# Optimization experiments

Measured on AMD Instinct MI355X. Metric: run time of the kernel, lower is better.

## Reference

```python
import math
import jax, jax.numpy as jnp
import numpy as np


def _expmap0(u):
    # geoopt Lorentz (k=1) expmap0 followed by projection back onto the hyperboloid.
    # Minkowski norm of the tangent input (geoopt clamps at 1e-8 before sqrt).
    u0 = u[..., :1]
    us = u[..., 1:]
    mink = -u0 * u0 + jnp.sum(us * us, axis=-1, keepdims=True)
    nomin = jnp.sqrt(jnp.maximum(mink, 1e-8))
    r = jnp.sinh(nomin) * u / nomin
    space = r[..., 1:]
    time = jnp.sqrt(1.0 + jnp.sum(space * space, axis=-1, keepdims=True))  # project()
    return jnp.concatenate([time, space], axis=-1)


def setup_inputs() -> dict:
    key = jax.random.key(0)
    B, T, E, H = 2, 1024, 1024, 16
    ks = jax.random.split(key, 8)
    s = 0.02
    return {
        "x": jax.random.normal(ks[0], (B, T, E), jnp.float32),
        "Wqkv": jax.random.normal(ks[1], (3 * E, E), jnp.float32) * s,
        "bqkv": jnp.zeros((3 * E,), jnp.float32),
        "Wout": jax.random.normal(ks[2], (E, E), jnp.float32) * s,
        "bout": jnp.zeros((E,), jnp.float32),
        "Wimp": jax.random.normal(ks[3], (1, E), jnp.float32) * s,
        "bimp": jnp.zeros((1,), jnp.float32),
        "Walpha": jax.random.normal(ks[4], (H, E), jnp.float32) * s,
        "balpha": jnp.zeros((H,), jnp.float32),
        "spike_threshold": jnp.asarray(0.5, jnp.float32),
        "log_k": jnp.full((H,), 0.54, jnp.float32),
        "qk_scale": jnp.asarray(0.1, jnp.float32),
    }


def reference(x, Wqkv, bqkv, Wout, bout, Wimp, bimp, Walpha, balpha,
              spike_threshold, log_k, qk_scale):
    B, T, C = x.shape
    H = log_k.shape[0]
    D = C // H

    importance = jax.nn.sigmoid(x @ Wimp.T + bimp)          # (B,T,1)
    # torch.tril on the (T,1) trailing dims keeps every element -> no-op mask.
    spikes = (importance > spike_threshold).astype(x.dtype)
    spike_mask = spikes.reshape(B, 1, T, 1)

    alpha = jax.nn.sigmoid(x @ Walpha.T + balpha)           # (B,T,H)
    alpha = jnp.transpose(alpha, (0, 2, 1))[..., None]      # (B,H,T,1)

    qkv = (x @ Wqkv.T + bqkv).reshape(B, T, 3, H, D)
    q = jnp.transpose(qkv[:, :, 0], (0, 2, 1, 3))           # (B,H,T,D)
    k = jnp.transpose(qkv[:, :, 1], (0, 2, 1, 3))
    v = jnp.transpose(qkv[:, :, 2], (0, 2, 1, 3))

    scores_euclid = jnp.einsum('bhtd,bhsd->bhts', q, k) / math.sqrt(D)

    safe_scale = jax.nn.sigmoid(qk_scale) * 1.5
    qn = q / jnp.maximum(jnp.linalg.norm(q, axis=-1, keepdims=True), 1e-12) * safe_scale
    kn = k / jnp.maximum(jnp.linalg.norm(k, axis=-1, keepdims=True), 1e-12) * safe_scale
    q_hyp = _expmap0(qn)
    k_hyp = _expmap0(kn)

    inner = (-jnp.einsum('bhti,bhsi->bhts', q_hyp[..., :1], k_hyp[..., :1])
             + jnp.einsum('bhtd,bhsd->bhts', q_hyp[..., 1:], k_hyp[..., 1:]))
    curv_k = (jax.nn.softplus(log_k) + 1e-6).reshape(1, H, 1, 1)
    mdot = jnp.maximum(-inner, 1.0 + 1e-6)
    dist = jnp.arccosh(mdot)
    scores_hyper = -(dist * dist) / curv_k

    scores = (1.0 - alpha) * scores_euclid + alpha * scores_hyper
    causal = jnp.tril(jnp.ones((T, T), bool))
    scores = jnp.where(causal[None, None], scores, -jnp.inf)

    attn = jax.nn.softmax(scores, axis=-1) * spike_mask     # dropout disabled (eval)
    y = jnp.einsum('bhts,bhsd->bhtd', attn, v)
    y = jnp.transpose(y, (0, 2, 1, 3)).reshape(B, T, C)
    return y @ Wout.T + bout
```

## Files before the change

### kernel.cpp

```cpp
#include <hip/hip_runtime.h>
#include <math.h>

#define B_ 2
#define T_ 1024
#define E_ 1024
#define H_ 16
#define D_ 64
#define M_ (B_*T_)

typedef __bf16 bf16x8 __attribute__((ext_vector_type(8)));
typedef __bf16 bf16x4 __attribute__((ext_vector_type(4)));
typedef float f32x4 __attribute__((ext_vector_type(4)));

__device__ __forceinline__ void* ldsp(__bf16* base, int row, int byte) {
  return (char*)base + row * 128 + (byte ^ ((row & 7) << 4));
}

__device__ __forceinline__ void gload_lds16(const void* g, void* l) {
  __builtin_amdgcn_global_load_lds((const __attribute__((address_space(1))) void*)g,
                                   (__attribute__((address_space(3))) void*)l, 16, 0, 0);
}

#define XV4 524288
#define WQV4 786432
#define WOV4 262144
#define TOTV4 (XV4 + WQV4 + WOV4)
__global__ __launch_bounds__(256) void conv_kernel(
    const float* __restrict__ x, const float* __restrict__ Wqkv,
    const float* __restrict__ Wout,
    __bf16* __restrict__ xb, __bf16* __restrict__ Wqkvb, __bf16* __restrict__ Woutb) {
  for (size_t i = (size_t)blockIdx.x * blockDim.x + threadIdx.x; i < TOTV4;
       i += (size_t)gridDim.x * blockDim.x) {
    const float4* src; __bf16* dst; size_t off;
    if (i < XV4)            { src = (const float4*)x;    dst = xb;    off = i; }
    else if (i < XV4+WQV4)  { src = (const float4*)Wqkv; dst = Wqkvb; off = i - XV4; }
    else                    { src = (const float4*)Wout; dst = Woutb; off = i - XV4 - WQV4; }
    float4 val = src[off];
    bf16x4 o = {(__bf16)val.x, (__bf16)val.y, (__bf16)val.z, (__bf16)val.w};
    *(bf16x4*)(dst + off * 4) = o;
  }
}

__global__ __launch_bounds__(256) void imp_alpha_kernel(
    const float* __restrict__ x,
    const float* __restrict__ Wimp, const float* __restrict__ bimp,
    const float* __restrict__ Walpha, const float* __restrict__ balpha,
    const float* __restrict__ thr_p,
    float* __restrict__ spike, float* __restrict__ alpha) {
  int m = blockIdx.x;
  int tid = threadIdx.x;
  const float* xr = x + (size_t)m * E_;
  float part[17];
#pragma unroll
  for (int i = 0; i < 17; ++i) part[i] = 0.f;
  for (int e = tid; e < E_; e += 256) {
    float xv = xr[e];
    part[16] += xv * Wimp[e];
#pragma unroll
    for (int h = 0; h < 16; ++h) part[h] += xv * Walpha[h * E_ + e];
  }
  __shared__ float red[17][4];
  int lane = tid & 63, wv = tid >> 6;
#pragma unroll
  for (int i = 0; i < 17; ++i) {
    float v = part[i];
    for (int off = 32; off > 0; off >>= 1) v += __shfl_down(v, off, 64);
    if (lane == 0) red[i][wv] = v;
  }
  __syncthreads();
  if (tid < 17) {
    float v = red[tid][0] + red[tid][1] + red[tid][2] + red[tid][3];
    if (tid == 16) {
      float z = v + bimp[0];
      float sig = 1.f / (1.f + expf(-z));
      spike[m] = (sig > thr_p[0]) ? 1.f : 0.f;
    } else {
      float z = v + balpha[tid];
      float a = 1.f / (1.f + expf(-z));
      int b = m >> 10, t = m & (T_ - 1);
      alpha[((size_t)(b * H_ + tid)) * T_ + t] = a;
    }
  }
}

__global__ __launch_bounds__(256) void qkv_gemm_kernel(
    const __bf16* __restrict__ A, const __bf16* __restrict__ Bm,
    const float* __restrict__ bias,
    __bf16* __restrict__ q, __bf16* __restrict__ k, __bf16* __restrict__ v) {
  __shared__ __bf16 As[128 * 32];
  __shared__ __bf16 Bs[128 * 32];
  const int K = E_;
  int tid = threadIdx.x;
  int w = tid >> 6, lane = tid & 63, lr = lane & 15, g = lane >> 4;
  int m0 = blockIdx.y * 128, n0 = blockIdx.x * 128;
  int wr = (w >> 1) * 64, wc = (w & 1) * 64;

  int task0 = tid, task1 = tid + 256;
  int r0s = task0 >> 2, c0s = task0 & 3;
  int r1s = task1 >> 2, c1s = task1 & 3;
  const __bf16* gA0 = A + (size_t)(m0 + r0s) * K + c0s * 8;
  const __bf16* gA1 = A + (size_t)(m0 + r1s) * K + c1s * 8;
  const __bf16* gB0 = Bm + (size_t)(n0 + r0s) * K + c0s * 8;
  const __bf16* gB1 = Bm + (size_t)(n0 + r1s) * K + c1s * 8;
  __bf16* lA0 = As + task0 * 8;
  __bf16* lA1 = As + task1 * 8;
  __bf16* lB0 = Bs + task0 * 8;
  __bf16* lB1 = Bs + task1 * 8;

  f32x4 acc[4][4];
#pragma unroll
  for (int i = 0; i < 4; ++i)
#pragma unroll
    for (int j = 0; j < 4; ++j) acc[i][j] = (f32x4){0.f, 0.f, 0.f, 0.f};

  for (int k0 = 0; k0 < K; k0 += 32) {
    gload_lds16(gA0, lA0); gload_lds16(gA1, lA1);
    gload_lds16(gB0, lB0); gload_lds16(gB1, lB1);
    gA0 += 32; gA1 += 32; gB0 += 32; gB1 += 32;
    __syncthreads();
    bf16x8 af[4], bf[4];
#pragma unroll
    for (int i = 0; i < 4; ++i) af[i] = *(bf16x8*)&As[(wr + i * 16 + lr) * 32 + g * 8];
#pragma unroll
    for (int j = 0; j < 4; ++j) bf[j] = *(bf16x8*)&Bs[(wc + j * 16 + lr) * 32 + g * 8];
#pragma unroll
    for (int i = 0; i < 4; ++i)
#pragma unroll
      for (int j = 0; j < 4; ++j)
        acc[i][j] = __builtin_amdgcn_mfma_f32_16x16x32_bf16(af[i], bf[j], acc[i][j], 0, 0, 0);
    __syncthreads();
  }

#pragma unroll
  for (int i = 0; i < 4; ++i) {
#pragma unroll
    for (int r = 0; r < 4; ++r) {
      int m = m0 + wr + i * 16 + g * 4 + r;
      int b = m >> 10, t = m & (T_ - 1);
#pragma unroll
      for (int j = 0; j < 4; ++j) {
        int n = n0 + wc + j * 16 + lr;
        float val = acc[i][j][r] + bias[n];
        int comp = n >> 10, h = (n >> 6) & 15, d = n & 63;
        __bf16* dst = (comp == 0) ? q : ((comp == 1) ? k : v);
        dst[(((size_t)(b * H_ + h)) * T_ + t) * 64 + d] = (__bf16)val;
      }
    }
  }
}

__global__ __launch_bounds__(256) void hyp_kernel(
    const __bf16* __restrict__ q, const __bf16* __restrict__ k,
    const float* __restrict__ qk_scale_p,
    __bf16* __restrict__ qh, __bf16* __restrict__ khn) {
  int wid = blockIdx.x * 4 + (threadIdx.x >> 6);
  int lane = threadIdx.x & 63;
  int is_k = wid >> 15;
  int row = wid & 32767;
  const __bf16* src = (is_k ? k : q) + (size_t)row * 64;
  float u = (float)src[lane];
  float nsq = u * u;
#pragma unroll
  for (int off = 32; off > 0; off >>= 1) nsq += __shfl_xor(nsq, off, 64);
  float norm = fmaxf(sqrtf(nsq), 1e-12f);
  float ss = 1.5f / (1.f + expf(-qk_scale_p[0]));
  float un = u / norm * ss;
  float s2 = un * un;
  float tot = s2;
#pragma unroll
  for (int off = 32; off > 0; off >>= 1) tot += __shfl_xor(tot, off, 64);
  float un0 = __shfl(un, 0, 64);
  float mink = tot - 2.f * un0 * un0;
  float nomin = sqrtf(fmaxf(mink, 1e-8f));
  float sc = sinhf(nomin) / nomin;
  float r = sc * un;
  float sp2 = (lane == 0) ? 0.f : r * r;
  float sps = sp2;
#pragma unroll
  for (int off = 32; off > 0; off >>= 1) sps += __shfl_xor(sps, off, 64);
  float tm = sqrtf(1.f + sps);
  float outv = (lane == 0) ? tm : r;
  if (is_k && lane != 0) outv = -outv;
  (is_k ? khn : qh)[(size_t)row * 64 + lane] = (__bf16)outv;
}

__global__ __launch_bounds__(256) void attn_kernel(
    const __bf16* __restrict__ q, const __bf16* __restrict__ k, const __bf16* __restrict__ v,
    const __bf16* __restrict__ qh, const __bf16* __restrict__ khn,
    const float* __restrict__ alpha, const float* __restrict__ log_k,
    __bf16* __restrict__ pacc, float* __restrict__ pml) {
  __shared__ __bf16 k_s[64 * 64];
  __shared__ __bf16 kh_s[64 * 64];
  __shared__ __bf16 vt_s[64 * 64];
  __shared__ __bf16 p_s[64 * 64];

  int bid = blockIdx.x;
  int bh = ((bid & 7) << 2) | ((bid >> 3) & 3);
  int rest = bid >> 5;
  int qt = rest & 15;
  int half = rest >> 4;
  int h = bh & 15;
  int t0 = qt * 64;
  int n_st = qt + 1;
  int nh = (n_st + 1) >> 1;
  int s_beg = half ? nh : 0;
  int s_end = half ? n_st : nh;

  int tid = threadIdx.x;
  int w = tid >> 6, lane = tid & 63;
  int lr = lane & 15, g = lane >> 4;
  int trow = w * 16;
  const size_t base = (size_t)bh * T_ * 64;

  const __bf16* qrow = q + base + (size_t)(t0 + trow + lr) * 64;
  const __bf16* qhrow = qh + base + (size_t)(t0 + trow + lr) * 64;
  bf16x8 aq0 = *(const bf16x8*)(qrow + g * 8);
  bf16x8 aq1 = *(const bf16x8*)(qrow + 32 + g * 8);
  bf16x8 ah0 = *(const bf16x8*)(qhrow + g * 8);
  bf16x8 ah1 = *(const bf16x8*)(qhrow + 32 + g * 8);

  float curv = log1pf(expf(log_k[h])) + 1e-6f;
  float hc = 0.69314718056f / curv;
  const float ec = 0.18033688f;
  int tg[4]; float al[4];
#pragma unroll
  for (int r = 0; r < 4; ++r) {
    tg[r] = t0 + trow + g * 4 + r;
    al[r] = alpha[(size_t)bh * T_ + tg[r]];
  }

  float m_r[4] = {-1e30f, -1e30f, -1e30f, -1e30f};
  float l_r[4] = {0.f, 0.f, 0.f, 0.f};
  f32x4 acc[4];
#pragma unroll
  for (int n = 0; n < 4; ++n) acc[n] = (f32x4){0.f, 0.f, 0.f, 0.f};

  for (int st = s_beg; st < s_end; ++st) {
    int s0 = st * 64;
    bool diag = (st == n_st - 1);
    __syncthreads();
#pragma unroll
    for (int it = 0; it < 2; ++it) {
      int task = tid + it * 256;
      int row = task >> 3, cj = task & 7;
      bf16x8 a = *(const bf16x8*)(k + base + (size_t)(s0 + row) * 64 + cj * 8);
      bf16x8 c = *(const bf16x8*)(khn + base + (size_t)(s0 + row) * 64 + cj * 8);
      *(bf16x8*)ldsp(k_s, row, cj * 16) = a;
      *(bf16x8*)ldsp(kh_s, row, cj * 16) = c;
    }
#pragma unroll
    for (int it = 0; it < 2; ++it) {
      int task = tid + it * 256;
      int srow = task & 63, dc = task >> 6;
      bf16x8 a = *(const bf16x8*)(v + base + (size_t)(s0 + srow) * 64 + dc * 8);
#pragma unroll
      for (int i = 0; i < 8; ++i)
        *(__bf16*)ldsp(vt_s, dc * 8 + i, srow * 2) = a[i];
    }
    __syncthreads();

    float pv[4][4];
    float pmax[4] = {-1e30f, -1e30f, -1e30f, -1e30f};
#pragma unroll
    for (int j = 0; j < 4; ++j) {
      if (diag && (s0 + j * 16 > t0 + trow + 15)) {
#pragma unroll
        for (int r = 0; r < 4; ++r) pv[j][r] = -1e30f;
        continue;
      }
      bf16x8 bk0 = *(bf16x8*)ldsp(k_s, j * 16 + lr, g * 16);
      bf16x8 bk1 = *(bf16x8*)ldsp(k_s, j * 16 + lr, 64 + g * 16);
      f32x4 z = {0.f, 0.f, 0.f, 0.f};
      z = __builtin_amdgcn_mfma_f32_16x16x32_bf16(aq0, bk0, z, 0, 0, 0);
      f32x4 se = __builtin_amdgcn_mfma_f32_16x16x32_bf16(aq1, bk1, z, 0, 0, 0);
      bf16x8 bh0 = *(bf16x8*)ldsp(kh_s, j * 16 + lr, g * 16);
      bf16x8 bh1 = *(bf16x8*)ldsp(kh_s, j * 16 + lr, 64 + g * 16);
      f32x4 z2 = {0.f, 0.f, 0.f, 0.f};
      z2 = __builtin_amdgcn_mfma_f32_16x16x32_bf16(ah0, bh0, z2, 0, 0, 0);
      f32x4 sh = __builtin_amdgcn_mfma_f32_16x16x32_bf16(ah1, bh1, z2, 0, 0, 0);
      int sg = s0 + j * 16 + lr;
#pragma unroll
      for (int r = 0; r < 4; ++r) {
        float sc_e = se[r] * ec;
        float md = fmaxf(sh[r], 1.0f + 1e-6f);
        float l2 = __log2f(md + sqrtf(fmaf(md, md, -1.f)));
        float t = fmaf(l2 * l2, hc, sc_e);
        float s = fmaf(-al[r], t, sc_e);
        if (diag && sg > tg[r]) s = -1e30f;
        pv[j][r] = s;
        pmax[r] = fmaxf(pmax[r], s);
      }
    }
#pragma unroll
    for (int r = 0; r < 4; ++r) {
      float mx = pmax[r];
      mx = fmaxf(mx, __shfl_xor(mx, 1, 64));
      mx = fmaxf(mx, __shfl_xor(mx, 2, 64));
      mx = fmaxf(mx, __shfl_xor(mx, 4, 64));
      mx = fmaxf(mx, __shfl_xor(mx, 8, 64));
      float mn = fmaxf(m_r[r], mx);
      float fac = exp2f(m_r[r] - mn);
      m_r[r] = mn;
      float ls = 0.f;
#pragma unroll
      for (int j = 0; j < 4; ++j) { pv[j][r] = exp2f(pv[j][r] - mn); ls += pv[j][r]; }
      ls += __shfl_xor(ls, 1, 64);
      ls += __shfl_xor(ls, 2, 64);
      ls += __shfl_xor(ls, 4, 64);
      ls += __shfl_xor(ls, 8, 64);
      l_r[r] = l_r[r] * fac + ls;
#pragma unroll
      for (int n = 0; n < 4; ++n) acc[n][r] *= fac;
    }
#pragma unroll
    for (int j = 0; j < 4; ++j)
#pragma unroll
      for (int r = 0; r < 4; ++r)
        *(__bf16*)ldsp(p_s, trow + g * 4 + r, (j * 16 + lr) * 2) = (__bf16)pv[j][r];
    bf16x8 ap0 = *(bf16x8*)ldsp(p_s, trow + lr, g * 16);
    bf16x8 ap1 = *(bf16x8*)ldsp(p_s, trow + lr, 64 + g * 16);
#pragma unroll
    for (int n = 0; n < 4; ++n) {
      bf16x8 bv0 = *(bf16x8*)ldsp(vt_s, n * 16 + lr, g * 16);
      bf16x8 bv1 = *(bf16x8*)ldsp(vt_s, n * 16 + lr, 64 + g * 16);
      acc[n] = __builtin_amdgcn_mfma_f32_16x16x32_bf16(ap0, bv0, acc[n], 0, 0, 0);
      acc[n] = __builtin_amdgcn_mfma_f32_16x16x32_bf16(ap1, bv1, acc[n], 0, 0, 0);
    }
  }

  int qt16 = (qt << 2) | w;
  int pidx = ((bh << 6) + qt16) * 2 + half;
  __bf16* pa = pacc + (size_t)pidx * 1024;
#pragma unroll
  for (int n = 0; n < 4; ++n)
#pragma unroll
    for (int r = 0; r < 4; ++r)
      pa[(g * 4 + r) * 64 + n * 16 + lr] = (__bf16)acc[n][r];
  if (lr == 0) {
#pragma unroll
    for (int r = 0; r < 4; ++r) {
      pml[(size_t)pidx * 32 + g * 4 + r] = m_r[r];
      pml[(size_t)pidx * 32 + 16 + g * 4 + r] = l_r[r];
    }
  }
}

__global__ __launch_bounds__(256) void merge_kernel(
    const __bf16* __restrict__ pacc, const float* __restrict__ pml,
    const float* __restrict__ spike, __bf16* __restrict__ yw) {
  int tid = threadIdx.x;
  int w = tid >> 6, lane = tid & 63;
  int wid = blockIdx.x * 4 + w;
  int bh = wid & 31;
  int qt = wid >> 5;
  int b = bh >> 4, h = bh & 15;
  size_t i1 = ((size_t)(bh << 6) + qt) * 2;
  size_t i2 = i1 + 1;
  const __bf16* a1 = pacc + i1 * 1024;
  const __bf16* a2 = pacc + i2 * 1024;
#pragma unroll 4
  for (int row = 0; row < 16; ++row) {
    float m1 = pml[i1 * 32 + row], l1 = pml[i1 * 32 + 16 + row];
    float m2 = pml[i2 * 32 + row], l2 = pml[i2 * 32 + 16 + row];
    float mm = fmaxf(m1, m2);
    float f1 = exp2f(m1 - mm), f2 = exp2f(m2 - mm);
    float l = l1 * f1 + l2 * f2;
    int t = qt * 16 + row;
    float iv = spike[(size_t)b * T_ + t] / l;
    float val = ((float)a1[row * 64 + lane] * f1 +
                 (float)a2[row * 64 + lane] * f2) * iv;
    yw[(size_t)(b * T_ + t) * E_ + h * 64 + lane] = (__bf16)val;
  }
}

__global__ __launch_bounds__(256) void out_gemm_kernel(
    const __bf16* __restrict__ A, const __bf16* __restrict__ Bm,
    const float* __restrict__ bias, float* __restrict__ outp) {
  __shared__ __bf16 As[128 * 32];
  __shared__ __bf16 Bs[128 * 32];
  const int K = E_;
  int tid = threadIdx.x;
  int w = tid >> 6, lane = tid & 63, lr = lane & 15, g = lane >> 4;
  int m0 = blockIdx.y * 128, n0 = blockIdx.x * 128;
  int wr = (w >> 1) * 64, wc = (w & 1) * 64;

  int task0 = tid, task1 = tid + 256;
  int r0s = task0 >> 2, c0s = task0 & 3;
  int r1s = task1 >> 2, c1s = task1 & 3;
  const __bf16* gA0 = A + (size_t)(m0 + r0s) * K + c0s * 8;
  const __bf16* gA1 = A + (size_t)(m0 + r1s) * K + c1s * 8;
  const __bf16* gB0 = Bm + (size_t)(n0 + r0s) * K + c0s * 8;
  const __bf16* gB1 = Bm + (size_t)(n0 + r1s) * K + c1s * 8;
  __bf16* lA0 = As + task0 * 8;
  __bf16* lA1 = As + task1 * 8;
  __bf16* lB0 = Bs + task0 * 8;
  __bf16* lB1 = Bs + task1 * 8;

  f32x4 acc[4][4];
#pragma unroll
  for (int i = 0; i < 4; ++i)
#pragma unroll
    for (int j = 0; j < 4; ++j) acc[i][j] = (f32x4){0.f, 0.f, 0.f, 0.f};

  for (int k0 = 0; k0 < K; k0 += 32) {
    gload_lds16(gA0, lA0); gload_lds16(gA1, lA1);
    gload_lds16(gB0, lB0); gload_lds16(gB1, lB1);
    gA0 += 32; gA1 += 32; gB0 += 32; gB1 += 32;
    __syncthreads();
    bf16x8 af[4], bf[4];
#pragma unroll
    for (int i = 0; i < 4; ++i) af[i] = *(bf16x8*)&As[(wr + i * 16 + lr) * 32 + g * 8];
#pragma unroll
    for (int j = 0; j < 4; ++j) bf[j] = *(bf16x8*)&Bs[(wc + j * 16 + lr) * 32 + g * 8];
#pragma unroll
    for (int i = 0; i < 4; ++i)
#pragma unroll
      for (int j = 0; j < 4; ++j)
        acc[i][j] = __builtin_amdgcn_mfma_f32_16x16x32_bf16(af[i], bf[j], acc[i][j], 0, 0, 0);
    __syncthreads();
  }

#pragma unroll
  for (int i = 0; i < 4; ++i) {
#pragma unroll
    for (int r = 0; r < 4; ++r) {
      int m = m0 + wr + i * 16 + g * 4 + r;
#pragma unroll
      for (int j = 0; j < 4; ++j) {
        int n = n0 + wc + j * 16 + lr;
        outp[(size_t)m * E_ + n] = acc[i][j][r] + bias[n];
      }
    }
  }
}

extern "C" void kernel_launch(void* const* d_in, const int* in_sizes, int n_in,
                              void* d_out, int out_size, void* d_ws, size_t ws_size,
                              hipStream_t stream) {
  const float* x      = (const float*)d_in[0];
  const float* Wqkv   = (const float*)d_in[1];
  const float* bqkv   = (const float*)d_in[2];
  const float* Wout   = (const float*)d_in[3];
  const float* bout   = (const float*)d_in[4];
  const float* Wimp   = (const float*)d_in[5];
  const float* bimp   = (const float*)d_in[6];
  const float* Walpha = (const float*)d_in[7];
  const float* balpha = (const float*)d_in[8];
  const float* thr    = (const float*)d_in[9];
  const float* log_k  = (const float*)d_in[10];
  const float* qk_sc  = (const float*)d_in[11];
  float* out = (float*)d_out;

  char* ws = (char*)d_ws;
  size_t off = 0;
  auto alloc = [&](size_t bytes) -> void* {
    void* p = (void*)(ws + off);
    off += (bytes + 255) & ~(size_t)255;
    return p;
  };
  const size_t qkv_elems = (size_t)B_ * H_ * T_ * D_;
  __bf16* xb    = (__bf16*)alloc((size_t)M_ * E_ * 2);
  __bf16* Wqkvb = (__bf16*)alloc((size_t)3 * E_ * E_ * 2);
  __bf16* Woutb = (__bf16*)alloc((size_t)E_ * E_ * 2);
  __bf16* q   = (__bf16*)alloc(qkv_elems * 2);
  __bf16* k   = (__bf16*)alloc(qkv_elems * 2);
  __bf16* v   = (__bf16*)alloc(qkv_elems * 2);
  __bf16* qh  = (__bf16*)alloc(qkv_elems * 2);
  __bf16* khn = (__bf16*)alloc(qkv_elems * 2);
  __bf16* yw  = (__bf16*)alloc((size_t)M_ * E_ * 2);
  float* alphaw = (float*)alloc((size_t)B_ * H_ * T_ * sizeof(float));
  float* spikew = (float*)alloc((size_t)M_ * sizeof(float));
  float* pml    = (float*)alloc((size_t)4096 * 32 * sizeof(float));
  __bf16* pacc = (__bf16*)ws;

  conv_kernel<<<1024, 256, 0, stream>>>(x, Wqkv, Wout, xb, Wqkvb, Woutb);
  imp_alpha_kernel<<<M_, 256, 0, stream>>>(x, Wimp, bimp, Walpha, balpha, thr,
                                           spikew, alphaw);
  qkv_gemm_kernel<<<dim3(24, 16), 256, 0, stream>>>(xb, Wqkvb, bqkv, q, k, v);
  hyp_kernel<<<(2 * B_ * H_ * T_) / 4, 256, 0, stream>>>(q, k, qk_sc, qh, khn);
  attn_kernel<<<1024, 256, 0, stream>>>(q, k, v, qh, khn, alphaw, log_k,
                                        pacc, pml);
  merge_kernel<<<512, 256, 0, stream>>>(pacc, pml, spikew, yw);
  out_gemm_kernel<<<dim3(8, 16), 256, 0, stream>>>(yw, Woutb, bout, out);
}
```

Before: 153.0 us.

## Derive hyperbolic inner product from Euclidean QK dot plus per-row scalars

New measurement: 165.0 us. 7.8% more time.

```diff
diff --git a/kernel.cpp b/kernel.cpp
--- a/kernel.cpp
+++ b/kernel.cpp
@@ -7,9 +7,11 @@
 #define H_ 16
 #define D_ 64
 #define M_ (B_*T_)
+#define SPLANE 32768
 
 typedef __bf16 bf16x8 __attribute__((ext_vector_type(8)));
 typedef __bf16 bf16x4 __attribute__((ext_vector_type(4)));
+typedef __bf16 bf16x2 __attribute__((ext_vector_type(2)));
 typedef float f32x4 __attribute__((ext_vector_type(4)));
 
 __device__ __forceinline__ void* ldsp(__bf16* base, int row, int byte) {
@@ -49,23 +51,25 @@
     float* __restrict__ spike, float* __restrict__ alpha) {
   int m = blockIdx.x;
   int tid = threadIdx.x;
-  const float* xr = x + (size_t)m * E_;
+  const float4* xr = (const float4*)(x + (size_t)m * E_);
+  float4 xv = xr[tid];
   float part[17];
-#pragma unroll
-  for (int i = 0; i < 17; ++i) part[i] = 0.f;
-  for (int e = tid; e < E_; e += 256) {
-    float xv = xr[e];
-    part[16] += xv * Wimp[e];
-#pragma unroll
-    for (int h = 0; h < 16; ++h) part[h] += xv * Walpha[h * E_ + e];
+  {
+    float4 wv = ((const float4*)Wimp)[tid];
+    part[16] = xv.x * wv.x + xv.y * wv.y + xv.z * wv.z + xv.w * wv.w;
+  }
+#pragma unroll
+  for (int h = 0; h < 16; ++h) {
+    float4 wv = ((const float4*)(Walpha + (size_t)h * E_))[tid];
+    part[h] = xv.x * wv.x + xv.y * wv.y + xv.z * wv.z + xv.w * wv.w;
   }
   __shared__ float red[17][4];
-  int lane = tid & 63, wv = tid >> 6;
+  int lane = tid & 63, wv_ = tid >> 6;
 #pragma unroll
   for (int i = 0; i < 17; ++i) {
     float v = part[i];
     for (int off = 32; off > 0; off >>= 1) v += __shfl_down(v, off, 64);
-    if (lane == 0) red[i][wv] = v;
+    if (lane == 0) red[i][wv_] = v;
   }
   __syncthreads();
   if (tid < 17) {
@@ -149,10 +153,10 @@
   }
 }
 
-__global__ __launch_bounds__(256) void hyp_kernel(
+__global__ __launch_bounds__(256) void scal_kernel(
     const __bf16* __restrict__ q, const __bf16* __restrict__ k,
     const float* __restrict__ qk_scale_p,
-    __bf16* __restrict__ qh, __bf16* __restrict__ khn) {
+    float* __restrict__ scalq, float* __restrict__ scalk) {
   int wid = blockIdx.x * 4 + (threadIdx.x >> 6);
   int lane = threadIdx.x & 63;
   int is_k = wid >> 15;
@@ -164,33 +168,28 @@
   for (int off = 32; off > 0; off >>= 1) nsq += __shfl_xor(nsq, off, 64);
   float norm = fmaxf(sqrtf(nsq), 1e-12f);
   float ss = 1.5f / (1.f + expf(-qk_scale_p[0]));
-  float un = u / norm * ss;
-  float s2 = un * un;
-  float tot = s2;
-#pragma unroll
-  for (int off = 32; off > 0; off >>= 1) tot += __shfl_xor(tot, off, 64);
-  float un0 = __shfl(un, 0, 64);
-  float mink = tot - 2.f * un0 * un0;
-  float nomin = sqrtf(fmaxf(mink, 1e-8f));
-  float sc = sinhf(nomin) / nomin;
-  float r = sc * un;
-  float sp2 = (lane == 0) ? 0.f : r * r;
-  float sps = sp2;
-#pragma unroll
-  for (int off = 32; off > 0; off >>= 1) sps += __shfl_xor(sps, off, 64);
-  float tm = sqrtf(1.f + sps);
-  float outv = (lane == 0) ? tm : r;
-  if (is_k && lane != 0) outv = -outv;
-  (is_k ? khn : qh)[(size_t)row * 64 + lane] = (__bf16)outv;
+  float row0 = __shfl(u, 0, 64);
+  float un0 = row0 / norm * ss;
+  float mink = ss * ss - 2.f * un0 * un0;
+  float nu = sqrtf(fmaxf(mink, 1e-8f));
+  float sc = sinhf(nu) / nu;
+  float Bv = sc * ss / norm;
+  float Av = sqrtf(1.f + sc * sc * (ss * ss - un0 * un0));
+  float Cv = Bv * row0;
+  if (lane == 0) {
+    float* dst = is_k ? scalk : scalq;
+    dst[row] = Av;
+    dst[SPLANE + row] = Bv;
+    dst[2 * SPLANE + row] = Cv;
+  }
 }
 
 __global__ __launch_bounds__(256) void attn_kernel(
     const __bf16* __restrict__ q, const __bf16* __restrict__ k, const __bf16* __restrict__ v,
-    const __bf16* __restrict__ qh, const __bf16* __restrict__ khn,
+    const float* __restrict__ scalq, const float* __restrict__ scalk,
     const float* __restrict__ alpha, const float* __restrict__ log_k,
     __bf16* __restrict__ pacc, float* __restrict__ pml) {
   __shared__ __bf16 k_s[64 * 64];
-  __shared__ __bf16 kh_s[64 * 64];
   __shared__ __bf16 vt_s[64 * 64];
   __shared__ __bf16 p_s[64 * 64];
 
@@ -213,20 +212,21 @@
   const size_t base = (size_t)bh * T_ * 64;
 
   const __bf16* qrow = q + base + (size_t)(t0 + trow + lr) * 64;
-  const __bf16* qhrow = qh + base + (size_t)(t0 + trow + lr) * 64;
   bf16x8 aq0 = *(const bf16x8*)(qrow + g * 8);
   bf16x8 aq1 = *(const bf16x8*)(qrow + 32 + g * 8);
-  bf16x8 ah0 = *(const bf16x8*)(qhrow + g * 8);
-  bf16x8 ah1 = *(const bf16x8*)(qhrow + 32 + g * 8);
 
   float curv = log1pf(expf(log_k[h])) + 1e-6f;
   float hc = 0.69314718056f / curv;
   const float ec = 0.18033688f;
-  int tg[4]; float al[4];
+  int tg[4]; float al[4], Aq[4], Bq[4], Cq[4];
 #pragma unroll
   for (int r = 0; r < 4; ++r) {
     tg[r] = t0 + trow + g * 4 + r;
+    int rowi = (bh << 10) + tg[r];
     al[r] = alpha[(size_t)bh * T_ + tg[r]];
+    Aq[r] = scalq[rowi];
+    Bq[r] = scalq[SPLANE + rowi];
+    Cq[r] = scalq[2 * SPLANE + rowi];
   }
 
   float m_r[4] = {-1e30f, -1e30f, -1e30f, -1e30f};
@@ -235,27 +235,27 @@
 #pragma unroll
   for (int n = 0; n < 4; ++n) acc[n] = (f32x4){0.f, 0.f, 0.f, 0.f};
 
+  int task0 = tid, task1 = tid + 256;
+  int row0s = task0 >> 3, cj0 = task0 & 7;
+  int row1s = task1 >> 3, cj1 = task1 & 7;
+  int s2 = tid & 31, dc = tid >> 5;
+
   for (int st = s_beg; st < s_end; ++st) {
     int s0 = st * 64;
     bool diag = (st == n_st - 1);
     __syncthreads();
-#pragma unroll
-    for (int it = 0; it < 2; ++it) {
-      int task = tid + it * 256;
-      int row = task >> 3, cj = task & 7;
-      bf16x8 a = *(const bf16x8*)(k + base + (size_t)(s0 + row) * 64 + cj * 8);
-      bf16x8 c = *(const bf16x8*)(khn + base + (size_t)(s0 + row) * 64 + cj * 8);
-      *(bf16x8*)ldsp(k_s, row, cj * 16) = a;
-      *(bf16x8*)ldsp(kh_s, row, cj * 16) = c;
-    }
-#pragma unroll
-    for (int it = 0; it < 2; ++it) {
-      int task = tid + it * 256;
-      int srow = task & 63, dc = task >> 6;
-      bf16x8 a = *(const bf16x8*)(v + base + (size_t)(s0 + srow) * 64 + dc * 8);
-#pragma unroll
-      for (int i = 0; i < 8; ++i)
-        *(__bf16*)ldsp(vt_s, dc * 8 + i, srow * 2) = a[i];
+    {
+      bf16x8 a0 = *(const bf16x8*)(k + base + (size_t)(s0 + row0s) * 64 + cj0 * 8);
+      bf16x8 a1 = *(const bf16x8*)(k + base + (size_t)(s0 + row1s) * 64 + cj1 * 8);
+      *(bf16x8*)ldsp(k_s, row0s, cj0 * 16) = a0;
+      *(bf16x8*)ldsp(k_s, row1s, cj1 * 16) = a1;
+      bf16x8 v0 = *(const bf16x8*)(v + base + (size_t)(s0 + 2 * s2) * 64 + dc * 8);
+      bf16x8 v1 = *(const bf16x8*)(v + base + (size_t)(s0 + 2 * s2 + 1) * 64 + dc * 8);
+#pragma unroll
+      for (int i = 0; i < 8; ++i) {
+        bf16x2 pr = {v0[i], v1[i]};
+        *(bf16x2*)ldsp(vt_s, dc * 8 + i, s2 * 4) = pr;
+      }
     }
     __syncthreads();
 
@@ -273,16 +273,17 @@
       f32x4 z = {0.f, 0.f, 0.f, 0.f};
       z = __builtin_amdgcn_mfma_f32_16x16x32_bf16(aq0, bk0, z, 0, 0, 0);
       f32x4 se = __builtin_amdgcn_mfma_f32_16x16x32_bf16(aq1, bk1, z, 0, 0, 0);
-      bf16x8 bh0 = *(bf16x8*)ldsp(kh_s, j * 16 + lr, g * 16);
-      bf16x8 bh1 = *(bf16x8*)ldsp(kh_s, j * 16 + lr, 64 + g * 16);
-      f32x4 z2 = {0.f, 0.f, 0.f, 0.f};
-      z2 = __builtin_amdgcn_mfma_f32_16x16x32_bf16(ah0, bh0, z2, 0, 0, 0);
-      f32x4 sh = __builtin_amdgcn_mfma_f32_16x16x32_bf16(ah1, bh1, z2, 0, 0, 0);
       int sg = s0 + j * 16 + lr;
+      int coli = (bh << 10) + sg;
+      float ak = scalk[coli];
+      float bk = scalk[SPLANE + coli];
+      float ck = scalk[2 * SPLANE + coli];
 #pragma unroll
       for (int r = 0; r < 4; ++r) {
-        float sc_e = se[r] * ec;
-        float md = fmaxf(sh[r], 1.0f + 1e-6f);
+        float dot = se[r];
+        float sc_e = dot * ec;
+        float md = fmaf(-Bq[r] * bk, dot, fmaf(Aq[r], ak, Cq[r] * ck));
+        md = fmaxf(md, 1.0f + 1e-6f);
         float l2 = __log2f(md + sqrtf(fmaf(md, md, -1.f)));
         float t = fmaf(l2 * l2, hc, sc_e);
         float s = fmaf(-al[r], t, sc_e);
@@ -465,20 +466,20 @@
   __bf16* q   = (__bf16*)alloc(qkv_elems * 2);
   __bf16* k   = (__bf16*)alloc(qkv_elems * 2);
   __bf16* v   = (__bf16*)alloc(qkv_elems * 2);
-  __bf16* qh  = (__bf16*)alloc(qkv_elems * 2);
-  __bf16* khn = (__bf16*)alloc(qkv_elems * 2);
   __bf16* yw  = (__bf16*)alloc((size_t)M_ * E_ * 2);
   float* alphaw = (float*)alloc((size_t)B_ * H_ * T_ * sizeof(float));
   float* spikew = (float*)alloc((size_t)M_ * sizeof(float));
   float* pml    = (float*)alloc((size_t)4096 * 32 * sizeof(float));
+  float* scalq  = (float*)alloc((size_t)3 * SPLANE * sizeof(float));
+  float* scalk  = (float*)alloc((size_t)3 * SPLANE * sizeof(float));
   __bf16* pacc = (__bf16*)ws;
 
   conv_kernel<<<1024, 256, 0, stream>>>(x, Wqkv, Wout, xb, Wqkvb, Woutb);
   imp_alpha_kernel<<<M_, 256, 0, stream>>>(x, Wimp, bimp, Walpha, balpha, thr,
                                            spikew, alphaw);
   qkv_gemm_kernel<<<dim3(24, 16), 256, 0, stream>>>(xb, Wqkvb, bqkv, q, k, v);
-  hyp_kernel<<<(2 * B_ * H_ * T_) / 4, 256, 0, stream>>>(q, k, qk_sc, qh, khn);
-  attn_kernel<<<1024, 256, 0, stream>>>(q, k, v, qh, khn, alphaw, log_k,
+  scal_kernel<<<(2 * B_ * H_ * T_) / 4, 256, 0, stream>>>(q, k, qk_sc, scalq, scalk);
+  attn_kernel<<<1024, 256, 0, stream>>>(q, k, v, scalq, scalk, alphaw, log_k,
                                         pacc, pml);
   merge_kernel<<<512, 256, 0, stream>>>(pacc, pml, spikew, yw);
   out_gemm_kernel<<<dim3(8, 16), 256, 0, stream>>>(yw, Woutb, bout, out);
```
